# Performance work log

Measured on AMD Instinct MI355X. Metric: run time of the kernel, lower is better.

The kernel has to match this reference:

```python
import jax, jax.numpy as jnp
import numpy as np

B, C, H, W = 8, 256, 64, 64
R = 8
CP = max(C // R, 3)  # C' = 32


def setup_inputs() -> dict:
    key = jax.random.key(0)
    ks = jax.random.split(key, 9)
    s_in = 1.0 / np.sqrt(C)
    s_cp = 1.0 / np.sqrt(CP)
    return {
        "x": jax.random.normal(ks[0], (B, C, H, W), dtype=jnp.float32),
        "Wq": jax.random.uniform(ks[1], (CP, C), minval=-s_in, maxval=s_in, dtype=jnp.float32),
        "bq": jax.random.uniform(ks[2], (CP,), minval=-s_in, maxval=s_in, dtype=jnp.float32),
        "Wk": jax.random.uniform(ks[3], (CP, C), minval=-s_in, maxval=s_in, dtype=jnp.float32),
        "bk": jax.random.uniform(ks[4], (CP,), minval=-s_in, maxval=s_in, dtype=jnp.float32),
        "Wv": jax.random.uniform(ks[5], (CP, C), minval=-s_in, maxval=s_in, dtype=jnp.float32),
        "bv": jax.random.uniform(ks[6], (CP,), minval=-s_in, maxval=s_in, dtype=jnp.float32),
        "Wb": jax.random.uniform(ks[7], (C, CP), minval=-s_cp, maxval=s_cp, dtype=jnp.float32),
        "bb": jax.random.uniform(ks[8], (C,), minval=-s_cp, maxval=s_cp, dtype=jnp.float32),
    }


def reference(x, Wq, bq, Wk, bk, Wv, bv, Wb, bb):
    b, c, h, w = x.shape
    n = h * w
    xf = x.reshape(b, c, n)  # [B, C, N]
    # 1x1 convs == channel-wise linear projections
    q = jnp.einsum('oc,bcn->bon', Wq, xf) + bq[None, :, None]  # [B, C', N]
    k = jnp.einsum('oc,bcn->bon', Wk, xf) + bk[None, :, None]
    v = jnp.einsum('oc,bcn->bon', Wv, xf) + bv[None, :, None]
    # attention: softmax(Q^T K) over last dim -> [B, N, N]
    attn = jax.nn.softmax(jnp.einsum('bon,bom->bnm', q, k), axis=-1)
    # out[b,c,i] = sum_j v[b,c,j] * attn[b,j,i]
    out = jnp.einsum('bcj,bji->bci', v, attn)  # [B, C', N]
    back = jnp.einsum('co,bon->bcn', Wb, out) + bb[None, :, None]  # [B, C, N]
    return back.reshape(b, c, h, w) + x
```

## Files before the change

kernel.cpp:

```cpp
#include <hip/hip_runtime.h>
#include <hip/hip_bf16.h>

#define NB 8
#define CC 256
#define CP 32
#define NN 4096
#define LOG2E 1.44269504088896340736f

typedef __attribute__((ext_vector_type(8))) short short8;
typedef __attribute__((ext_vector_type(4))) float floatx4;
typedef __attribute__((ext_vector_type(4))) int intx4;

static __device__ __forceinline__ ushort bf16r(float f) {
    __hip_bfloat16 h = __float2bfloat16(f);
    return *reinterpret_cast<ushort*>(&h);
}
static __device__ __forceinline__ float bf2f(ushort u) {
    union { unsigned int i; float f; } x;
    x.i = ((unsigned int)u) << 16;
    return x.f;
}
static __device__ __forceinline__ short8 load_frag(const ushort* p) {
    intx4 v = *reinterpret_cast<const intx4*>(p);
    return *reinterpret_cast<short8*>(&v);
}
static __device__ __forceinline__ unsigned int pk2(float a, float b) {
#if defined(__has_builtin) && __has_builtin(__builtin_amdgcn_perm)
    return __builtin_amdgcn_perm(__float_as_uint(b) + 0x8000u, __float_as_uint(a) + 0x8000u, 0x07060302u);
#else
    unsigned int ua = __float_as_uint(a) + 0x8000u;
    unsigned int ub = __float_as_uint(b) + 0x8000u;
    return (ua >> 16) | (ub & 0xFFFF0000u);
#endif
}
static __device__ __forceinline__ ushort pk1(float a) {
    return (ushort)((__float_as_uint(a) + 0x8000u) >> 16);
}
static __device__ __forceinline__ float fexp2(float x) {
#if defined(__has_builtin)
#if __has_builtin(__builtin_amdgcn_exp2f)
    return __builtin_amdgcn_exp2f(x);
#else
    return __expf(x * 0.69314718055994530942f);
#endif
#else
    return __expf(x * 0.69314718055994530942f);
#endif
}

__global__ void prep_w(const float* __restrict__ Wq, const float* __restrict__ Wk,
                       const float* __restrict__ Wv, const float* __restrict__ Wb,
                       ushort* __restrict__ W96, ushort* __restrict__ W2b) {
    int r = blockIdx.x, c = threadIdx.x;
    if (r < 96) {
        const float* src = (r < 32) ? (Wq + r * CC) : ((r < 64) ? (Wk + (r - 32) * CC) : (Wv + (r - 64) * CC));
        float scale = (r < 32) ? LOG2E : 1.0f;
        W96[r * CC + c] = bf16r(src[c] * scale);
    } else {
        int idx = (r - 96) * 256 + c;
        W2b[idx] = bf16r(Wb[idx]);
    }
}

__global__ __launch_bounds__(256) void proj_kernel(
    const float* __restrict__ x, const ushort* __restrict__ W96,
    const float* __restrict__ bq, const float* __restrict__ bk, const float* __restrict__ bv,
    ushort* __restrict__ Qt, ushort* __restrict__ Kt, ushort* __restrict__ Vt) {
    __shared__ ushort xt[64 * 264];
    int b = blockIdx.x >> 6, nt = blockIdx.x & 63;
    int t = threadIdx.x;
    int n0 = nt * 64;
    {
        int cq = t >> 4, n4 = (t & 15) * 4;
#pragma unroll
        for (int cc = 0; cc < 4; cc++) {
            int c_base = cc * 64 + cq * 4;
            float4 xv[4];
#pragma unroll
            for (int e = 0; e < 4; e++)
                xv[e] = *reinterpret_cast<const float4*>(&x[((size_t)b * CC + c_base + e) * NN + n0 + n4]);
            const float* xs = reinterpret_cast<const float*>(xv);
#pragma unroll
            for (int jj = 0; jj < 4; jj++) {
                ushort4 u;
                u.x = pk1(xs[0 * 4 + jj]);
                u.y = pk1(xs[1 * 4 + jj]);
                u.z = pk1(xs[2 * 4 + jj]);
                u.w = pk1(xs[3 * 4 + jj]);
                *reinterpret_cast<ushort4*>(&xt[(n4 + jj) * 264 + c_base]) = u;
            }
        }
    }
    __syncthreads();
    int w = t >> 6, lane = t & 63, l15 = lane & 15, q = lane >> 4;
    floatx4 acc[6];
#pragma unroll
    for (int k = 0; k < 6; k++) acc[k] = (floatx4){0.f, 0.f, 0.f, 0.f};
#pragma unroll
    for (int ks = 0; ks < 8; ks++) {
        short8 bfrag = load_frag(&xt[(w * 16 + l15) * 264 + ks * 32 + q * 8]);
#pragma unroll
        for (int ot = 0; ot < 6; ot++) {
            short8 afrag = load_frag(&W96[(size_t)(ot * 16 + l15) * CC + ks * 32 + q * 8]);
            acc[ot] = __builtin_amdgcn_mfma_f32_16x16x32_bf16(afrag, bfrag, acc[ot], 0, 0, 0);
        }
    }
    int n = n0 + w * 16 + l15;
#pragma unroll
    for (int ot = 0; ot < 6; ot++) {
        const float* bias = (ot < 2) ? bq : ((ot < 4) ? bk : bv);
        ushort* dst = (ot < 2) ? Qt : ((ot < 4) ? Kt : Vt);
        int o0 = (ot & 1) * 16 + q * 4;
        float4 b4 = *reinterpret_cast<const float4*>(bias + o0);
        float sc = (ot < 2) ? LOG2E : 1.0f;
        ushort4 pk;
        pk.x = bf16r(acc[ot][0] + b4.x * sc);
        pk.y = bf16r(acc[ot][1] + b4.y * sc);
        pk.z = bf16r(acc[ot][2] + b4.z * sc);
        pk.w = bf16r(acc[ot][3] + b4.w * sc);
        *reinterpret_cast<ushort4*>(&dst[((size_t)b * NN + n) * CP + o0]) = pk;
    }
}

__global__ __launch_bounds__(256, 4) void passA_kernel(
    const ushort* __restrict__ Qt, const ushort* __restrict__ Kt, float* __restrict__ Fp) {
    __shared__ ushort kst[256 * 40];
    int bid = blockIdx.x;
    int mq = bid & 3, jt = (bid >> 2) & 63, b = bid >> 8;
    int w = threadIdx.x >> 6, lane = threadIdx.x & 63;
    int l15 = lane & 15, q = lane >> 4;
    int j = jt * 64 + w * 16 + l15;

    short8 af = load_frag(&Qt[((size_t)b * NN + j) * CP + q * 8]);
    floatx4 lacc = (floatx4){0.f, 0.f, 0.f, 0.f};

    for (int mc = 0; mc < 4; mc++) {
        int m0 = mq * 1024 + mc * 256;
        __syncthreads();
        {
            const intx4* src = reinterpret_cast<const intx4*>(&Kt[((size_t)b * NN + m0) * CP]);
            intx4* dst = reinterpret_cast<intx4*>(kst);
#pragma unroll
            for (int s = 0; s < 4; s++) {
                int g = threadIdx.x + 256 * s;
                dst[(g >> 2) * 5 + (g & 3)] = src[g];
            }
        }
        __syncthreads();
#pragma unroll
        for (int ms = 0; ms < 16; ms++) {
            short8 bf = load_frag(&kst[(ms * 16 + l15) * 40 + q * 8]);
            floatx4 z = (floatx4){0.f, 0.f, 0.f, 0.f};
            floatx4 s = __builtin_amdgcn_mfma_f32_16x16x32_bf16(af, bf, z, 0, 0, 0);
            lacc[0] += fexp2(s[0]);
            lacc[1] += fexp2(s[1]);
            lacc[2] += fexp2(s[2]);
            lacc[3] += fexp2(s[3]);
        }
    }
#pragma unroll
    for (int d = 1; d < 16; d <<= 1) {
        lacc[0] += __shfl_xor(lacc[0], d, 64);
        lacc[1] += __shfl_xor(lacc[1], d, 64);
        lacc[2] += __shfl_xor(lacc[2], d, 64);
        lacc[3] += __shfl_xor(lacc[3], d, 64);
    }
    if (l15 == 0) {
        float4 f4;
        f4.x = lacc[0]; f4.y = lacc[1]; f4.z = lacc[2]; f4.w = lacc[3];
        *reinterpret_cast<float4*>(&Fp[((size_t)mq * NB + b) * NN + jt * 64 + w * 16 + q * 4]) = f4;
    }
}

__global__ __launch_bounds__(256) void fold_kernel(
    const ushort* __restrict__ Vt, const float* __restrict__ Fp, ushort* __restrict__ Vp) {
    __shared__ ushort tile[32 * 136];
    const size_t PL = (size_t)NB * NN;
    int b = blockIdx.x >> 5, nc = blockIdx.x & 31;
    int t = threadIdx.x;
    int half = t >> 7, nl = t & 127;
    int n = nc * 128 + nl;
    size_t bn = (size_t)b * NN + n;
    float f = 1.0f / (Fp[bn] + Fp[PL + bn] + Fp[2 * PL + bn] + Fp[3 * PL + bn]);
    const ushort* src = &Vt[bn * CP + half * 16];
#pragma unroll
    for (int g = 0; g < 2; g++) {
        intx4 raw = *reinterpret_cast<const intx4*>(src + g * 8);
        const ushort* us = reinterpret_cast<const ushort*>(&raw);
#pragma unroll
        for (int e = 0; e < 8; e++) {
            tile[(half * 16 + g * 8 + e) * 136 + nl] = pk1(bf2f(us[e]) * f);
        }
    }
    __syncthreads();
#pragma unroll
    for (int cc = 0; cc < 16; cc++) {
        int c = half * 16 + cc;
        Vp[((size_t)b * CP + c) * NN + nc * 128 + nl] = tile[c * 136 + nl];
    }
}

__global__ __launch_bounds__(256, 6) void passB_kernel(
    const ushort* __restrict__ Qt, const ushort* __restrict__ Kt, const ushort* __restrict__ Vp,
    const ushort* __restrict__ W2b, const float* __restrict__ bb, const float* __restrict__ x,
    float* __restrict__ out) {
    __shared__ float olds4[4 * 32 * 33];

    int bid = blockIdx.x;
    int it = bid & 127, b = bid >> 7;
    int w = threadIdx.x >> 6, lane = threadIdx.x & 63;
    int l15 = lane & 15, q = lane >> 4;
    int i0 = it * 32;

    short8 kf0 = load_frag(&Kt[((size_t)b * NN + i0 + l15) * CP + q * 8]);
    short8 kf1 = load_frag(&Kt[((size_t)b * NN + i0 + 16 + l15) * CP + q * 8]);

    floatx4 acc00 = (floatx4){0.f, 0.f, 0.f, 0.f};
    floatx4 acc10 = (floatx4){0.f, 0.f, 0.f, 0.f};
    floatx4 acc01 = (floatx4){0.f, 0.f, 0.f, 0.f};
    floatx4 acc11 = (floatx4){0.f, 0.f, 0.f, 0.f};

    int qrow = (l15 >> 2) * 8 + (l15 & 3);
    const ushort* qbase = Qt + ((size_t)b * NN + qrow) * CP + q * 8;
    const ushort* vbase0 = Vp + ((size_t)b * CP + l15) * NN + q * 8;
    const ushort* vbase1 = Vp + ((size_t)b * CP + 16 + l15) * NN + q * 8;

#pragma unroll 2
    for (int jb = w; jb < 128; jb += 4) {
        int j0 = jb * 32;
        short8 a0 = load_frag(qbase + (size_t)j0 * CP);
        short8 a1 = load_frag(qbase + (size_t)(j0 + 4) * CP);
        short8 va0 = load_frag(vbase0 + j0);
        short8 va1 = load_frag(vbase1 + j0);

        floatx4 z = (floatx4){0.f, 0.f, 0.f, 0.f};
        floatx4 s0A = __builtin_amdgcn_mfma_f32_16x16x32_bf16(a0, kf0, z, 0, 0, 0);
        floatx4 s1A = __builtin_amdgcn_mfma_f32_16x16x32_bf16(a1, kf0, z, 0, 0, 0);
        floatx4 s0B = __builtin_amdgcn_mfma_f32_16x16x32_bf16(a0, kf1, z, 0, 0, 0);
        floatx4 s1B = __builtin_amdgcn_mfma_f32_16x16x32_bf16(a1, kf1, z, 0, 0, 0);

        union { intx4 v; short8 s; } wa, wb2;
        wa.v.x = pk2(fexp2(s0A[0]), fexp2(s0A[1]));
        wa.v.y = pk2(fexp2(s0A[2]), fexp2(s0A[3]));
        wa.v.z = pk2(fexp2(s1A[0]), fexp2(s1A[1]));
        wa.v.w = pk2(fexp2(s1A[2]), fexp2(s1A[3]));
        wb2.v.x = pk2(fexp2(s0B[0]), fexp2(s0B[1]));
        wb2.v.y = pk2(fexp2(s0B[2]), fexp2(s0B[3]));
        wb2.v.z = pk2(fexp2(s1B[0]), fexp2(s1B[1]));
        wb2.v.w = pk2(fexp2(s1B[2]), fexp2(s1B[3]));

        acc00 = __builtin_amdgcn_mfma_f32_16x16x32_bf16(va0, wa.s, acc00, 0, 0, 0);
        acc10 = __builtin_amdgcn_mfma_f32_16x16x32_bf16(va1, wa.s, acc10, 0, 0, 0);
        acc01 = __builtin_amdgcn_mfma_f32_16x16x32_bf16(va0, wb2.s, acc01, 0, 0, 0);
        acc11 = __builtin_amdgcn_mfma_f32_16x16x32_bf16(va1, wb2.s, acc11, 0, 0, 0);
    }

    int mbase = w * (32 * 33);
#pragma unroll
    for (int r = 0; r < 4; r++) {
        olds4[mbase + (q * 4 + r) * 33 + l15] = acc00[r];
        olds4[mbase + (16 + q * 4 + r) * 33 + l15] = acc10[r];
        olds4[mbase + (q * 4 + r) * 33 + 16 + l15] = acc01[r];
        olds4[mbase + (16 + q * 4 + r) * 33 + 16 + l15] = acc11[r];
    }
    __syncthreads();

    short8 bfr[2];
#pragma unroll
    for (int s = 0; s < 2; s++) {
        float o8[8];
#pragma unroll
        for (int jj = 0; jj < 8; jj++) {
            int o = q * 8 + jj;
            int idx = o * 33 + s * 16 + l15;
            o8[jj] = olds4[idx] + olds4[1056 + idx] + olds4[2112 + idx] + olds4[3168 + idx];
        }
        union { intx4 v; short8 sh; } u;
        u.v.x = pk2(o8[0], o8[1]);
        u.v.y = pk2(o8[2], o8[3]);
        u.v.z = pk2(o8[4], o8[5]);
        u.v.w = pk2(o8[6], o8[7]);
        bfr[s] = u.sh;
    }
    int c0 = w * 64;
#pragma unroll
    for (int cs = 0; cs < 4; cs++) {
        short8 af = load_frag(&W2b[(size_t)(c0 + cs * 16 + l15) * CP + q * 8]);
#pragma unroll
        for (int s = 0; s < 2; s++) {
            floatx4 z = (floatx4){0.f, 0.f, 0.f, 0.f};
            floatx4 d = __builtin_amdgcn_mfma_f32_16x16x32_bf16(af, bfr[s], z, 0, 0, 0);
#pragma unroll
            for (int r = 0; r < 4; r++) {
                int c = c0 + cs * 16 + q * 4 + r;
                int i = i0 + s * 16 + l15;
                size_t idx = ((size_t)b * CC + c) * NN + i;
                out[idx] = d[r] + bb[c] + x[idx];
            }
        }
    }
}

extern "C" void kernel_launch(void* const* d_in, const int* in_sizes, int n_in,
                              void* d_out, int out_size, void* d_ws, size_t ws_size,
                              hipStream_t stream) {
    const float* x  = (const float*)d_in[0];
    const float* Wq = (const float*)d_in[1];
    const float* bq = (const float*)d_in[2];
    const float* Wk = (const float*)d_in[3];
    const float* bk = (const float*)d_in[4];
    const float* Wv = (const float*)d_in[5];
    const float* bv = (const float*)d_in[6];
    const float* Wb = (const float*)d_in[7];
    const float* bb = (const float*)d_in[8];
    float* out = (float*)d_out;

    char* ws = (char*)d_ws;
    ushort* Qt  = (ushort*)(ws);
    ushort* Kt  = (ushort*)(ws + (2u << 20));
    ushort* Vp  = (ushort*)(ws + (4u << 20));
    ushort* Vt  = (ushort*)(ws + (6u << 20));
    float*  Fp  = (float*) (ws + (8u << 20));
    ushort* W96 = (ushort*)(ws + (8u << 20) + (1u << 19));
    ushort* W2b = (ushort*)(ws + (8u << 20) + (1u << 19) + (48u << 10));

    prep_w<<<128, 256, 0, stream>>>(Wq, Wk, Wv, Wb, W96, W2b);
    proj_kernel<<<512, 256, 0, stream>>>(x, W96, bq, bk, bv, Qt, Kt, Vt);
    passA_kernel<<<2048, 256, 0, stream>>>(Qt, Kt, Fp);
    fold_kernel<<<256, 256, 0, stream>>>(Vt, Fp, Vp);
    passB_kernel<<<1024, 256, 0, stream>>>(Qt, Kt, Vp, W2b, bb, x, out);
}
```

Before: 182.1 us.

## Restructure passA without LDS staging and prefetch fragments in passA and passB

passA no longer stages K tiles in shared memory with barriers. Each wave now holds four Q fragments (64 query rows) in registers and streams its own 256 K rows straight from global memory, prefetching the next K fragment. A small LDS reduction then combines the partial row sums from the four waves. passB software-pipelines the Q and V fragment loads one iteration ahead and lowers its occupancy hint from 6 to 4 to leave room for the extra live registers. This targets load latency and barrier stalls, but it raises register pressure and means each wave re-reads K from global memory or cache.

```diff
diff --git a/kernel.cpp b/kernel.cpp
--- a/kernel.cpp
+++ b/kernel.cpp
@@ -122,53 +122,63 @@
     }
 }
 
-__global__ __launch_bounds__(256, 4) void passA_kernel(
+__global__ __launch_bounds__(256, 6) void passA_kernel(
     const ushort* __restrict__ Qt, const ushort* __restrict__ Kt, float* __restrict__ Fp) {
-    __shared__ ushort kst[256 * 40];
+    __shared__ float red[4][64];
     int bid = blockIdx.x;
     int mq = bid & 3, jt = (bid >> 2) & 63, b = bid >> 8;
     int w = threadIdx.x >> 6, lane = threadIdx.x & 63;
     int l15 = lane & 15, q = lane >> 4;
-    int j = jt * 64 + w * 16 + l15;
-
-    short8 af = load_frag(&Qt[((size_t)b * NN + j) * CP + q * 8]);
-    floatx4 lacc = (floatx4){0.f, 0.f, 0.f, 0.f};
-
-    for (int mc = 0; mc < 4; mc++) {
-        int m0 = mq * 1024 + mc * 256;
-        __syncthreads();
-        {
-            const intx4* src = reinterpret_cast<const intx4*>(&Kt[((size_t)b * NN + m0) * CP]);
-            intx4* dst = reinterpret_cast<intx4*>(kst);
-#pragma unroll
-            for (int s = 0; s < 4; s++) {
-                int g = threadIdx.x + 256 * s;
-                dst[(g >> 2) * 5 + (g & 3)] = src[g];
-            }
-        }
-        __syncthreads();
-#pragma unroll
-        for (int ms = 0; ms < 16; ms++) {
-            short8 bf = load_frag(&kst[(ms * 16 + l15) * 40 + q * 8]);
-            floatx4 z = (floatx4){0.f, 0.f, 0.f, 0.f};
-            floatx4 s = __builtin_amdgcn_mfma_f32_16x16x32_bf16(af, bf, z, 0, 0, 0);
-            lacc[0] += fexp2(s[0]);
-            lacc[1] += fexp2(s[1]);
-            lacc[2] += fexp2(s[2]);
-            lacc[3] += fexp2(s[3]);
-        }
-    }
-#pragma unroll
-    for (int d = 1; d < 16; d <<= 1) {
-        lacc[0] += __shfl_xor(lacc[0], d, 64);
-        lacc[1] += __shfl_xor(lacc[1], d, 64);
-        lacc[2] += __shfl_xor(lacc[2], d, 64);
-        lacc[3] += __shfl_xor(lacc[3], d, 64);
+
+    short8 af[4];
+#pragma unroll
+    for (int js = 0; js < 4; js++)
+        af[js] = load_frag(&Qt[((size_t)b * NN + jt * 64 + js * 16 + l15) * CP + q * 8]);
+
+    floatx4 lacc[4];
+#pragma unroll
+    for (int js = 0; js < 4; js++) lacc[js] = (floatx4){0.f, 0.f, 0.f, 0.f};
+
+    const ushort* kbase = Kt + ((size_t)b * NN + mq * 1024 + w * 256 + l15) * CP + q * 8;
+    short8 bfc = load_frag(kbase);
+
+#pragma unroll 2
+    for (int ms = 0; ms < 16; ms++) {
+        int mn = (ms + 1) & 15;
+        short8 bfn = load_frag(kbase + (size_t)(mn * 16) * CP);
+        floatx4 z = (floatx4){0.f, 0.f, 0.f, 0.f};
+#pragma unroll
+        for (int js = 0; js < 4; js++) {
+            floatx4 s = __builtin_amdgcn_mfma_f32_16x16x32_bf16(af[js], bfc, z, 0, 0, 0);
+            lacc[js][0] += fexp2(s[0]);
+            lacc[js][1] += fexp2(s[1]);
+            lacc[js][2] += fexp2(s[2]);
+            lacc[js][3] += fexp2(s[3]);
+        }
+        bfc = bfn;
+    }
+#pragma unroll
+    for (int js = 0; js < 4; js++) {
+#pragma unroll
+        for (int d = 1; d < 16; d <<= 1) {
+            lacc[js][0] += __shfl_xor(lacc[js][0], d, 64);
+            lacc[js][1] += __shfl_xor(lacc[js][1], d, 64);
+            lacc[js][2] += __shfl_xor(lacc[js][2], d, 64);
+            lacc[js][3] += __shfl_xor(lacc[js][3], d, 64);
+        }
     }
     if (l15 == 0) {
-        float4 f4;
-        f4.x = lacc[0]; f4.y = lacc[1]; f4.z = lacc[2]; f4.w = lacc[3];
-        *reinterpret_cast<float4*>(&Fp[((size_t)mq * NB + b) * NN + jt * 64 + w * 16 + q * 4]) = f4;
+#pragma unroll
+        for (int js = 0; js < 4; js++) {
+#pragma unroll
+            for (int r = 0; r < 4; r++) red[w][js * 16 + q * 4 + r] = lacc[js][r];
+        }
+    }
+    __syncthreads();
+    int t = threadIdx.x;
+    if (t < 64) {
+        float s = red[0][t] + red[1][t] + red[2][t] + red[3][t];
+        Fp[((size_t)mq * NB + b) * NN + jt * 64 + t] = s;
     }
 }
 
@@ -200,7 +210,7 @@
     }
 }
 
-__global__ __launch_bounds__(256, 6) void passB_kernel(
+__global__ __launch_bounds__(256, 4) void passB_kernel(
     const ushort* __restrict__ Qt, const ushort* __restrict__ Kt, const ushort* __restrict__ Vp,
     const ushort* __restrict__ W2b, const float* __restrict__ bb, const float* __restrict__ x,
     float* __restrict__ out) {
@@ -225,19 +235,25 @@
     const ushort* vbase0 = Vp + ((size_t)b * CP + l15) * NN + q * 8;
     const ushort* vbase1 = Vp + ((size_t)b * CP + 16 + l15) * NN + q * 8;
 
+    int jf = w * 32;
+    short8 a0c = load_frag(qbase + (size_t)jf * CP);
+    short8 a1c = load_frag(qbase + (size_t)(jf + 4) * CP);
+    short8 va0c = load_frag(vbase0 + jf);
+    short8 va1c = load_frag(vbase1 + jf);
+
 #pragma unroll 2
     for (int jb = w; jb < 128; jb += 4) {
-        int j0 = jb * 32;
-        short8 a0 = load_frag(qbase + (size_t)j0 * CP);
-        short8 a1 = load_frag(qbase + (size_t)(j0 + 4) * CP);
-        short8 va0 = load_frag(vbase0 + j0);
-        short8 va1 = load_frag(vbase1 + j0);
+        int jn0 = ((jb + 4) & 127) * 32;
+        short8 a0n = load_frag(qbase + (size_t)jn0 * CP);
+        short8 a1n = load_frag(qbase + (size_t)(jn0 + 4) * CP);
+        short8 va0n = load_frag(vbase0 + jn0);
+        short8 va1n = load_frag(vbase1 + jn0);
 
         floatx4 z = (floatx4){0.f, 0.f, 0.f, 0.f};
-        floatx4 s0A = __builtin_amdgcn_mfma_f32_16x16x32_bf16(a0, kf0, z, 0, 0, 0);
-        floatx4 s1A = __builtin_amdgcn_mfma_f32_16x16x32_bf16(a1, kf0, z, 0, 0, 0);
-        floatx4 s0B = __builtin_amdgcn_mfma_f32_16x16x32_bf16(a0, kf1, z, 0, 0, 0);
-        floatx4 s1B = __builtin_amdgcn_mfma_f32_16x16x32_bf16(a1, kf1, z, 0, 0, 0);
+        floatx4 s0A = __builtin_amdgcn_mfma_f32_16x16x32_bf16(a0c, kf0, z, 0, 0, 0);
+        floatx4 s1A = __builtin_amdgcn_mfma_f32_16x16x32_bf16(a1c, kf0, z, 0, 0, 0);
+        floatx4 s0B = __builtin_amdgcn_mfma_f32_16x16x32_bf16(a0c, kf1, z, 0, 0, 0);
+        floatx4 s1B = __builtin_amdgcn_mfma_f32_16x16x32_bf16(a1c, kf1, z, 0, 0, 0);
 
         union { intx4 v; short8 s; } wa, wb2;
         wa.v.x = pk2(fexp2(s0A[0]), fexp2(s0A[1]));
@@ -249,10 +265,12 @@
         wb2.v.z = pk2(fexp2(s1B[0]), fexp2(s1B[1]));
         wb2.v.w = pk2(fexp2(s1B[2]), fexp2(s1B[3]));
 
-        acc00 = __builtin_amdgcn_mfma_f32_16x16x32_bf16(va0, wa.s, acc00, 0, 0, 0);
-        acc10 = __builtin_amdgcn_mfma_f32_16x16x32_bf16(va1, wa.s, acc10, 0, 0, 0);
-        acc01 = __builtin_amdgcn_mfma_f32_16x16x32_bf16(va0, wb2.s, acc01, 0, 0, 0);
-        acc11 = __builtin_amdgcn_mfma_f32_16x16x32_bf16(va1, wb2.s, acc11, 0, 0, 0);
+        acc00 = __builtin_amdgcn_mfma_f32_16x16x32_bf16(va0c, wa.s, acc00, 0, 0, 0);
+        acc10 = __builtin_amdgcn_mfma_f32_16x16x32_bf16(va1c, wa.s, acc10, 0, 0, 0);
+        acc01 = __builtin_amdgcn_mfma_f32_16x16x32_bf16(va0c, wb2.s, acc01, 0, 0, 0);
+        acc11 = __builtin_amdgcn_mfma_f32_16x16x32_bf16(va1c, wb2.s, acc11, 0, 0, 0);
+
+        a0c = a0n; a1c = a1n; va0c = va0n; va1c = va1n;
     }
 
     int mbase = w * (32 * 33);
```

Result: no change. 180.3 us (-1.0%).
